# Performance work log

Measured on AMD Instinct MI355X. Metric: run time of the kernel, lower is better.

Reference implementation:

```python
import jax, jax.numpy as jnp
import numpy as np

B, T, D, Q = 32, 2048, 512, 512


def setup_inputs() -> dict:
    key = jax.random.key(0)
    k0, k1, k2, k3, k4, k5 = jax.random.split(key, 6)
    output_data = jax.random.normal(k0, (B, T, D), dtype=jnp.float32)
    query = jax.random.normal(k1, (B, Q), dtype=jnp.float32)
    # valid lengths in [1, T] so no row is fully masked
    lengths = jax.random.randint(k2, (B,), 1, T + 1).astype(jnp.int32)
    w = jax.random.normal(k3, (D, D), dtype=jnp.float32) * (1.0 / np.sqrt(D))
    u = jax.random.normal(k4, (D, Q), dtype=jnp.float32) * (1.0 / np.sqrt(Q))
    v = jax.random.normal(k5, (D, 1), dtype=jnp.float32)
    return {"output_data": output_data, "query": query, "lengths": lengths,
            "w": w, "u": u, "v": v}


def reference(output_data, query, lengths, w, u, v):
    # raw_score = W @ output + U @ query (broadcast over seq)   [B, T, D]
    raw = jnp.einsum('btd,ed->bte', output_data, w) \
        + jnp.einsum('bq,eq->be', query, u)[:, None, :]
    # score = tanh(raw) @ v                                     [B, T, 1]
    score = jnp.tanh(raw) @ v
    # additive mask: 0 on valid positions, -inf on padding
    valid = jnp.arange(T)[None, :] < lengths[:, None]           # [B, T]
    score = score + jnp.where(valid, 0.0, -jnp.inf)[:, :, None]
    weights = jax.nn.softmax(score, axis=1)                     # [B, T, 1]
    expectation = jnp.sum(weights * output_data, axis=1)        # [B, D]
    # dropout_rate=0.0 -> dropout is identity
    return score, weights, expectation
```

## Files before the change

kernel.cpp:

```cpp
#include <hip/hip_runtime.h>
#include <math.h>


#define TPB 256
constexpr int B = 32, T = 2048, D = 512, Qd = 512;
constexpr int NROW = B * T;
#define NEG_SENTINEL (-1e30f)

typedef __attribute__((ext_vector_type(8))) short bf16x8;
typedef __attribute__((ext_vector_type(4))) float f32x4;

__device__ __forceinline__ void lds_barrier() {
    asm volatile("s_waitcnt lgkmcnt(0)" ::: "memory");
    __builtin_amdgcn_s_barrier();
}

__device__ __forceinline__ unsigned cvtpk(float a, float b) {
    unsigned r;
    asm("v_cvt_pk_bf16_f32 %0, %1, %2" : "=v"(r) : "v"(a), "v"(b));
    return r;
}
__device__ __forceinline__ unsigned packsplit(float f0, float f1, unsigned& lopack) {
    unsigned hp = cvtpk(f0, f1);
    float h0 = __builtin_bit_cast(float, hp << 16);
    float h1 = __builtin_bit_cast(float, hp & 0xFFFF0000u);
    lopack = cvtpk(f0 - h0, f1 - h1);
    return hp;
}
__device__ __forceinline__ void cvt8(const float4 a, const float4 b, uint4& hi, uint4& lo) {
    hi.x = packsplit(a.x, a.y, lo.x);
    hi.y = packsplit(a.z, a.w, lo.y);
    hi.z = packsplit(b.x, b.y, lo.z);
    hi.w = packsplit(b.z, b.w, lo.w);
}
__device__ __forceinline__ float fast_tanh(float x) {
    float a = fabsf(x);
    float e = __expf(-2.f * a);
    float t = (1.f - e) / (1.f + e);
    return copysignf(t, x);
}

__global__ void k_uq(const float* __restrict__ query, const float* __restrict__ u,
                     float* __restrict__ uq) {
    int b = blockIdx.x;
    __shared__ float q_s[Qd];
    for (int i = threadIdx.x; i < Qd; i += TPB) q_s[i] = query[b * Qd + i];
    __syncthreads();
    for (int e = threadIdx.x; e < D; e += TPB) {
        const float4* urow = (const float4*)(u + (size_t)e * Qd);
        float acc = 0.f;
        for (int q4 = 0; q4 < Qd / 4; ++q4) {
            float4 uu = urow[q4];
            float4 qq = *(const float4*)(q_s + q4 * 4);
            acc += uu.x * qq.x + uu.y * qq.y + uu.z * qq.z + uu.w * qq.w;
        }
        uq[b * D + e] = acc;
    }
}

__global__ void k_convW(const float* __restrict__ W,
                        uint4* __restrict__ WhF, uint4* __restrict__ WlF) {
    const int g = blockIdx.x * 256 + threadIdx.x;
    const int e = g >> 6, s = g & 63;
    const float4* src = (const float4*)(W + (size_t)e * D + s * 8);
    float4 a = src[0], bq = src[1];
    uint4 hi, lo;
    cvt8(a, bq, hi, lo);
    const int nt = e >> 7, cb = (e >> 4) & 7, lo16 = e & 15;
    const int kc = s >> 2, hi4 = s & 3;
    const size_t idx = ((size_t)(nt * 16 + kc) * 8 + cb) * 64 + hi4 * 16 + lo16;
    WhF[idx] = hi;
    WlF[idx] = lo;
}

__global__ __launch_bounds__(256, 4) void k_gemm(
    const float* __restrict__ X,
    const uint4* __restrict__ WhF,
    const uint4* __restrict__ WlF,
    const float* __restrict__ v,
    const float* __restrict__ uqg,
    float* __restrict__ partialS)
{
    __shared__ uint4 Ah[2][4 * 128], Al[2][4 * 128];
    __shared__ float scr[2][128];

    const int gidx = blockIdx.x;
    const int logical = (gidx & 7) * 256 + (gidx >> 3);
    const int mt = logical >> 2, nt = logical & 3;
    const int row0 = mt * 128, e0 = nt * 128;
    const int b = row0 >> 11;

    const int tid = threadIdx.x, lane = tid & 63, wid = tid >> 6;
    const int wm = wid >> 1, wn = wid & 1;
    const int lo16 = lane & 15, hi4 = lane >> 4;
    const int arow = tid & 127, akh = tid >> 7;

    const float4* Xg = (const float4*)(X + (size_t)(row0 + arow) * D + akh * 16);
    const uint4* WhB = WhF + ((size_t)nt * 16) * 8 * 64 + (wn * 4) * 64 + lane;
    const uint4* WlB = WlF + ((size_t)nt * 16) * 8 * 64 + (wn * 4) * 64 + lane;

    f32x4 acc[4][4];
#pragma unroll
    for (int i = 0; i < 4; ++i)
#pragma unroll
        for (int j = 0; j < 4; ++j) acc[i][j] = (f32x4){0.f, 0.f, 0.f, 0.f};

    float4 xr[2][4];
#pragma unroll
    for (int i = 0; i < 4; ++i) xr[0][i] = Xg[i];
#pragma unroll
    for (int i = 0; i < 4; ++i) xr[1][i] = Xg[8 + i];
    {
        uint4 hp, lp;
        cvt8(xr[0][0], xr[0][1], hp, lp);
        Ah[0][(akh * 2 + 0) * 128 + arow] = hp;
        Al[0][(akh * 2 + 0) * 128 + arow] = lp;
        cvt8(xr[0][2], xr[0][3], hp, lp);
        Ah[0][(akh * 2 + 1) * 128 + arow] = hp;
        Al[0][(akh * 2 + 1) * 128 + arow] = lp;
    }

#pragma unroll
    for (int kc = 0; kc < 16; ++kc) {
        const int cur = kc & 1, nxt = cur ^ 1;
        lds_barrier();

        uint4 bhr[4], blr[4];
        {
            const uint4* wh = WhB + (size_t)kc * 8 * 64;
            const uint4* wl = WlB + (size_t)kc * 8 * 64;
#pragma unroll
            for (int fc = 0; fc < 4; ++fc) {
                bhr[fc] = wh[fc * 64];
                blr[fc] = wl[fc * 64];
            }
        }

        if (kc + 1 < 16) {
            uint4 hp, lp;
            cvt8(xr[nxt][0], xr[nxt][1], hp, lp);
            Ah[nxt][(akh * 2 + 0) * 128 + arow] = hp;
            Al[nxt][(akh * 2 + 0) * 128 + arow] = lp;
            cvt8(xr[nxt][2], xr[nxt][3], hp, lp);
            Ah[nxt][(akh * 2 + 1) * 128 + arow] = hp;
            Al[nxt][(akh * 2 + 1) * 128 + arow] = lp;
        }

        bf16x8 aH[4], aL[4];
#pragma unroll
        for (int fr = 0; fr < 4; ++fr) {
            const int idx = hi4 * 128 + wm * 64 + fr * 16 + lo16;
            aH[fr] = __builtin_bit_cast(bf16x8, Ah[cur][idx]);
            aL[fr] = __builtin_bit_cast(bf16x8, Al[cur][idx]);
        }

#pragma unroll
        for (int fc = 0; fc < 4; ++fc) {
            const bf16x8 bH = __builtin_bit_cast(bf16x8, bhr[fc]);
            const bf16x8 bL = __builtin_bit_cast(bf16x8, blr[fc]);
#pragma unroll
            for (int fr = 0; fr < 4; ++fr) {
                acc[fr][fc] = __builtin_amdgcn_mfma_f32_16x16x32_bf16(aH[fr], bH, acc[fr][fc], 0, 0, 0);
                acc[fr][fc] = __builtin_amdgcn_mfma_f32_16x16x32_bf16(aH[fr], bL, acc[fr][fc], 0, 0, 0);
                acc[fr][fc] = __builtin_amdgcn_mfma_f32_16x16x32_bf16(aL[fr], bH, acc[fr][fc], 0, 0, 0);
            }
        }

        if (kc + 2 < 16) {
#pragma unroll
            for (int i = 0; i < 4; ++i) xr[cur][i] = Xg[(kc + 2) * 8 + i];
        }
    }

    const int colbase = e0 + wn * 64;
#pragma unroll
    for (int fr = 0; fr < 4; ++fr) {
        float ps[4] = {0.f, 0.f, 0.f, 0.f};
#pragma unroll
        for (int fc = 0; fc < 4; ++fc) {
            const int col = colbase + fc * 16 + lo16;
            const float uqc = uqg[b * D + col];
            const float vc  = v[col];
#pragma unroll
            for (int i = 0; i < 4; ++i)
                ps[i] += fast_tanh(acc[fr][fc][i] + uqc) * vc;
        }
#pragma unroll
        for (int i = 0; i < 4; ++i) {
            float p = ps[i];
#pragma unroll
            for (int off = 8; off >= 1; off >>= 1) p += __shfl_xor(p, off, 16);
            if (lo16 == 0) scr[wn][wm * 64 + fr * 16 + hi4 * 4 + i] = p;
        }
    }
    __syncthreads();
    if (tid < 128)
        partialS[(size_t)nt * NROW + row0 + tid] = scr[0][tid] + scr[1][tid];
}

__global__ void k_combine(const float* __restrict__ partialS,
                          const int* __restrict__ lengths,
                          float* __restrict__ score) {
    const int i = blockIdx.x * TPB + threadIdx.x;
    const int b = i >> 11, t = i & (T - 1);
    float s = partialS[i] + partialS[NROW + i] + partialS[2 * NROW + i] + partialS[3 * NROW + i];
    score[i] = (t < lengths[b]) ? s : NEG_SENTINEL;
}

__global__ void k_softmax(const float* __restrict__ score, float* __restrict__ weights) {
    const int b = blockIdx.x;
    const float* s = score + (size_t)b * T;
    float m = -INFINITY;
    for (int t = threadIdx.x; t < T; t += TPB) m = fmaxf(m, s[t]);
#pragma unroll
    for (int off = 32; off >= 1; off >>= 1) m = fmaxf(m, __shfl_xor(m, off, 64));
    __shared__ float redm[4];
    if ((threadIdx.x & 63) == 0) redm[threadIdx.x >> 6] = m;
    __syncthreads();
    m = fmaxf(fmaxf(redm[0], redm[1]), fmaxf(redm[2], redm[3]));

    float sum = 0.f;
    for (int t = threadIdx.x; t < T; t += TPB) sum += __expf(s[t] - m);
#pragma unroll
    for (int off = 32; off >= 1; off >>= 1) sum += __shfl_xor(sum, off, 64);
    __shared__ float reds[4];
    if ((threadIdx.x & 63) == 0) reds[threadIdx.x >> 6] = sum;
    __syncthreads();
    const float inv = 1.f / (reds[0] + reds[1] + reds[2] + reds[3]);

    for (int t = threadIdx.x; t < T; t += TPB)
        weights[(size_t)b * T + t] = __expf(s[t] - m) * inv;
}

__global__ void k_exp_partial(const float* __restrict__ X, const float* __restrict__ wts,
                              float* __restrict__ part) {
    const int b = blockIdx.x >> 4;
    const int c = blockIdx.x & 15;
    const int t0 = c * 128;
    const int d0 = threadIdx.x * 4;
    const float* Xb = X + ((size_t)b * T + t0) * D + d0;
    const float* wb = wts + (size_t)b * T + t0;
    float4 a = {0.f, 0.f, 0.f, 0.f};
    for (int t = 0; t < 128; ++t) {
        const float wgt = wb[t];
        const float4 x = *(const float4*)(Xb + (size_t)t * D);
        a.x += wgt * x.x; a.y += wgt * x.y; a.z += wgt * x.z; a.w += wgt * x.w;
    }
    *(float4*)(part + ((size_t)(b * 16 + c)) * D + d0) = a;
}

__global__ void k_exp_reduce(const float* __restrict__ part, float* __restrict__ out) {
    const int i = blockIdx.x * TPB + threadIdx.x;
    const int b = i >> 9, d = i & 511;
    float a = 0.f;
#pragma unroll
    for (int c = 0; c < 16; ++c) a += part[((size_t)(b * 16 + c)) * D + d];
    out[i] = a;
}

extern "C" void kernel_launch(void* const* d_in, const int* in_sizes, int n_in,
                              void* d_out, int out_size, void* d_ws, size_t ws_size,
                              hipStream_t stream) {
    const float* X      = (const float*)d_in[0];
    const float* query  = (const float*)d_in[1];
    const int*   len    = (const int*)  d_in[2];
    const float* w      = (const float*)d_in[3];
    const float* u      = (const float*)d_in[4];
    const float* v      = (const float*)d_in[5];

    float* out     = (float*)d_out;
    float* score   = out;
    float* weights = out + (size_t)B * T;
    float* expec   = out + (size_t)2 * B * T;

    float* uq       = (float*)d_ws;
    float* partialS = uq + (size_t)B * D;
    uint4* WhF      = (uint4*)(partialS + (size_t)4 * NROW);
    uint4* WlF      = WhF + 32768;
    float* part     = partialS;

    k_uq         <<<B,            TPB, 0, stream>>>(query, u, uq);
    k_convW      <<<128,          TPB, 0, stream>>>(w, WhF, WlF);
    k_gemm       <<<2048,         TPB, 0, stream>>>(X, WhF, WlF, v, uq, partialS);
    k_combine    <<<NROW / TPB,   TPB, 0, stream>>>(partialS, len, score);
    k_softmax    <<<B,            TPB, 0, stream>>>(score, weights);
    k_exp_partial<<<B * 16,       128, 0, stream>>>(X, weights, part);
    k_exp_reduce <<<B * D / TPB,  TPB, 0, stream>>>(part, expec);
}
```

Baseline: 185.7 us.

## Stage W fragments through LDS with register prefetch and reorder MFMA pipeline

Each block now loads its W hi/lo tile for the next k-chunk cooperatively into registers, then writes it to shared memory after compute. Previously each wave read its own W fragments straight from global memory. A second barrier separates fragment reads from compute, the MFMAs are regrouped by product term, and s_setprio raises wave priority around the MFMA block. Launch bounds drop to 3 blocks per SM to make room for the extra registers and LDS, which costs occupancy and adds a barrier per iteration.

Result: slower. 326.8 us (+76.0%).

```diff
diff --git a/kernel.cpp b/kernel.cpp
--- a/kernel.cpp
+++ b/kernel.cpp
@@ -73,7 +73,7 @@
     WlF[idx] = lo;
 }
 
-__global__ __launch_bounds__(256, 4) void k_gemm(
+__global__ __launch_bounds__(256, 3) void k_gemm(
     const float* __restrict__ X,
     const uint4* __restrict__ WhF,
     const uint4* __restrict__ WlF,
@@ -82,6 +82,7 @@
     float* __restrict__ partialS)
 {
     __shared__ uint4 Ah[2][4 * 128], Al[2][4 * 128];
+    __shared__ uint4 Bh[8 * 64], Bl[8 * 64];
     __shared__ float scr[2][128];
 
     const int gidx = blockIdx.x;
@@ -96,8 +97,8 @@
     const int arow = tid & 127, akh = tid >> 7;
 
     const float4* Xg = (const float4*)(X + (size_t)(row0 + arow) * D + akh * 16);
-    const uint4* WhB = WhF + ((size_t)nt * 16) * 8 * 64 + (wn * 4) * 64 + lane;
-    const uint4* WlB = WlF + ((size_t)nt * 16) * 8 * 64 + (wn * 4) * 64 + lane;
+    const uint4* WhS = WhF + ((size_t)nt * 16) * 8 * 64 + tid;
+    const uint4* WlS = WlF + ((size_t)nt * 16) * 8 * 64 + tid;
 
     f32x4 acc[4][4];
 #pragma unroll
@@ -110,6 +111,9 @@
     for (int i = 0; i < 4; ++i) xr[0][i] = Xg[i];
 #pragma unroll
     for (int i = 0; i < 4; ++i) xr[1][i] = Xg[8 + i];
+    uint4 bs0, bs1, bs2, bs3;
+    bs0 = WhS[0];  bs1 = WhS[256];
+    bs2 = WlS[0];  bs3 = WlS[256];
     {
         uint4 hp, lp;
         cvt8(xr[0][0], xr[0][1], hp, lp);
@@ -119,21 +123,37 @@
         Ah[0][(akh * 2 + 1) * 128 + arow] = hp;
         Al[0][(akh * 2 + 1) * 128 + arow] = lp;
     }
+    Bh[tid] = bs0;  Bh[tid + 256] = bs1;
+    Bl[tid] = bs2;  Bl[tid + 256] = bs3;
 
 #pragma unroll
     for (int kc = 0; kc < 16; ++kc) {
         const int cur = kc & 1, nxt = cur ^ 1;
         lds_barrier();
 
-        uint4 bhr[4], blr[4];
-        {
-            const uint4* wh = WhB + (size_t)kc * 8 * 64;
-            const uint4* wl = WlB + (size_t)kc * 8 * 64;
-#pragma unroll
-            for (int fc = 0; fc < 4; ++fc) {
-                bhr[fc] = wh[fc * 64];
-                blr[fc] = wl[fc * 64];
-            }
+        bf16x8 aH[4], aL[4], bH[4], bL[4];
+#pragma unroll
+        for (int fr = 0; fr < 4; ++fr) {
+            const int idx = hi4 * 128 + wm * 64 + fr * 16 + lo16;
+            aH[fr] = __builtin_bit_cast(bf16x8, Ah[cur][idx]);
+            aL[fr] = __builtin_bit_cast(bf16x8, Al[cur][idx]);
+        }
+#pragma unroll
+        for (int fc = 0; fc < 4; ++fc) {
+            const int idx = (wn * 4 + fc) * 64 + lane;
+            bH[fc] = __builtin_bit_cast(bf16x8, Bh[idx]);
+            bL[fc] = __builtin_bit_cast(bf16x8, Bl[idx]);
+        }
+
+        if (kc + 1 < 16) {
+            const uint4* wh = WhS + (size_t)(kc + 1) * 512;
+            const uint4* wl = WlS + (size_t)(kc + 1) * 512;
+            bs0 = wh[0];  bs1 = wh[256];
+            bs2 = wl[0];  bs3 = wl[256];
+        }
+        if (kc + 2 < 16) {
+#pragma unroll
+            for (int i = 0; i < 4; ++i) xr[cur][i] = Xg[(kc + 2) * 8 + i];
         }
 
         if (kc + 1 < 16) {
@@ -146,29 +166,29 @@
             Al[nxt][(akh * 2 + 1) * 128 + arow] = lp;
         }
 
-        bf16x8 aH[4], aL[4];
-#pragma unroll
-        for (int fr = 0; fr < 4; ++fr) {
-            const int idx = hi4 * 128 + wm * 64 + fr * 16 + lo16;
-            aH[fr] = __builtin_bit_cast(bf16x8, Ah[cur][idx]);
-            aL[fr] = __builtin_bit_cast(bf16x8, Al[cur][idx]);
-        }
-
-#pragma unroll
-        for (int fc = 0; fc < 4; ++fc) {
-            const bf16x8 bH = __builtin_bit_cast(bf16x8, bhr[fc]);
-            const bf16x8 bL = __builtin_bit_cast(bf16x8, blr[fc]);
-#pragma unroll
-            for (int fr = 0; fr < 4; ++fr) {
-                acc[fr][fc] = __builtin_amdgcn_mfma_f32_16x16x32_bf16(aH[fr], bH, acc[fr][fc], 0, 0, 0);
-                acc[fr][fc] = __builtin_amdgcn_mfma_f32_16x16x32_bf16(aH[fr], bL, acc[fr][fc], 0, 0, 0);
-                acc[fr][fc] = __builtin_amdgcn_mfma_f32_16x16x32_bf16(aL[fr], bH, acc[fr][fc], 0, 0, 0);
-            }
-        }
-
-        if (kc + 2 < 16) {
-#pragma unroll
-            for (int i = 0; i < 4; ++i) xr[cur][i] = Xg[(kc + 2) * 8 + i];
+        lds_barrier();
+
+        __builtin_amdgcn_s_setprio(1);
+#pragma unroll
+        for (int fc = 0; fc < 4; ++fc)
+#pragma unroll
+            for (int fr = 0; fr < 4; ++fr)
+                acc[fr][fc] = __builtin_amdgcn_mfma_f32_16x16x32_bf16(aH[fr], bH[fc], acc[fr][fc], 0, 0, 0);
+#pragma unroll
+        for (int fc = 0; fc < 4; ++fc)
+#pragma unroll
+            for (int fr = 0; fr < 4; ++fr)
+                acc[fr][fc] = __builtin_amdgcn_mfma_f32_16x16x32_bf16(aH[fr], bL[fc], acc[fr][fc], 0, 0, 0);
+#pragma unroll
+        for (int fc = 0; fc < 4; ++fc)
+#pragma unroll
+            for (int fr = 0; fr < 4; ++fr)
+                acc[fr][fc] = __builtin_amdgcn_mfma_f32_16x16x32_bf16(aL[fr], bH[fc], acc[fr][fc], 0, 0, 0);
+        __builtin_amdgcn_s_setprio(0);
+
+        if (kc + 1 < 16) {
+            Bh[tid] = bs0;  Bh[tid + 256] = bs1;
+            Bl[tid] = bs2;  Bl[tid + 256] = bs3;
         }
     }
 
```

## Pre-split X into bf16 hi/lo fragment layout and stream GEMM from registers

Applied to the files above, without the earlier changes.

Adds a conversion kernel that splits X into bf16 hi/lo parts and stores them in MFMA fragment order in workspace. A new GEMM kernel then loads A and B fragments straight from global memory into double-buffered registers, with no LDS staging. The aim is to remove the in-GEMM conversion and the LDS traffic and barriers. In exchange it writes and rereads a 128 MB intermediate for X, and occupancy drops to 2 blocks per CU. The new path runs only if the workspace is large enough, otherwise the old kernel is used.

Result: slower. 205.9 us (+10.9%).

```diff
diff --git a/kernel.cpp b/kernel.cpp
--- a/kernel.cpp
+++ b/kernel.cpp
@@ -73,6 +73,114 @@
     WlF[idx] = lo;
 }
 
+__global__ void k_convX(const float* __restrict__ X,
+                        uint4* __restrict__ XhF, uint4* __restrict__ XlF) {
+    const int g = blockIdx.x * 256 + threadIdx.x;
+    const int lo16 = g & 15, hi4 = (g >> 4) & 3, rb = (g >> 6) & 7;
+    const int kc = (g >> 9) & 15, mt = g >> 13;
+    const int row = mt * 128 + rb * 16 + lo16;
+    const int d0 = kc * 32 + hi4 * 8;
+    const float4* src = (const float4*)(X + (size_t)row * D + d0);
+    float4 a = src[0], bq = src[1];
+    uint4 hi, lo;
+    cvt8(a, bq, hi, lo);
+    XhF[g] = hi;
+    XlF[g] = lo;
+}
+
+__global__ __launch_bounds__(256, 2) void k_gemm_stream(
+    const uint4* __restrict__ XhF, const uint4* __restrict__ XlF,
+    const uint4* __restrict__ WhF, const uint4* __restrict__ WlF,
+    const float* __restrict__ v,
+    const float* __restrict__ uqg,
+    float* __restrict__ partialS)
+{
+    __shared__ float scr[2][128];
+
+    const int gidx = blockIdx.x;
+    const int logical = (gidx & 7) * 256 + (gidx >> 3);
+    const int mt = logical >> 2, nt = logical & 3;
+    const int row0 = mt * 128, e0 = nt * 128;
+    const int b = row0 >> 11;
+
+    const int tid = threadIdx.x, lane = tid & 63, wid = tid >> 6;
+    const int wm = wid >> 1, wn = wid & 1;
+    const int lo16 = lane & 15, hi4 = lane >> 4;
+
+    const uint4* XhB = XhF + ((size_t)mt * 16) * 8 * 64 + (wm * 4) * 64 + lane;
+    const uint4* XlB = XlF + ((size_t)mt * 16) * 8 * 64 + (wm * 4) * 64 + lane;
+    const uint4* WhB = WhF + ((size_t)nt * 16) * 8 * 64 + (wn * 4) * 64 + lane;
+    const uint4* WlB = WlF + ((size_t)nt * 16) * 8 * 64 + (wn * 4) * 64 + lane;
+
+    f32x4 acc[4][4];
+#pragma unroll
+    for (int i = 0; i < 4; ++i)
+#pragma unroll
+        for (int j = 0; j < 4; ++j) acc[i][j] = (f32x4){0.f, 0.f, 0.f, 0.f};
+
+    uint4 ah[2][4], al[2][4], bh[2][4], bl[2][4];
+#pragma unroll
+    for (int f = 0; f < 4; ++f) {
+        ah[0][f] = XhB[f * 64];
+        al[0][f] = XlB[f * 64];
+        bh[0][f] = WhB[f * 64];
+        bl[0][f] = WlB[f * 64];
+    }
+
+#pragma unroll
+    for (int kc = 0; kc < 16; ++kc) {
+        const int cur = kc & 1, nxt = cur ^ 1;
+        if (kc + 1 < 16) {
+            const size_t off = (size_t)(kc + 1) * 512;
+#pragma unroll
+            for (int f = 0; f < 4; ++f) {
+                ah[nxt][f] = XhB[off + f * 64];
+                al[nxt][f] = XlB[off + f * 64];
+                bh[nxt][f] = WhB[off + f * 64];
+                bl[nxt][f] = WlB[off + f * 64];
+            }
+        }
+#pragma unroll
+        for (int fc = 0; fc < 4; ++fc) {
+            const bf16x8 bH = __builtin_bit_cast(bf16x8, bh[cur][fc]);
+            const bf16x8 bL = __builtin_bit_cast(bf16x8, bl[cur][fc]);
+#pragma unroll
+            for (int fr = 0; fr < 4; ++fr) {
+                const bf16x8 aH = __builtin_bit_cast(bf16x8, ah[cur][fr]);
+                const bf16x8 aL = __builtin_bit_cast(bf16x8, al[cur][fr]);
+                acc[fr][fc] = __builtin_amdgcn_mfma_f32_16x16x32_bf16(aH, bH, acc[fr][fc], 0, 0, 0);
+                acc[fr][fc] = __builtin_amdgcn_mfma_f32_16x16x32_bf16(aH, bL, acc[fr][fc], 0, 0, 0);
+                acc[fr][fc] = __builtin_amdgcn_mfma_f32_16x16x32_bf16(aL, bH, acc[fr][fc], 0, 0, 0);
+            }
+        }
+    }
+
+    const int colbase = e0 + wn * 64;
+#pragma unroll
+    for (int fr = 0; fr < 4; ++fr) {
+        float ps[4] = {0.f, 0.f, 0.f, 0.f};
+#pragma unroll
+        for (int fc = 0; fc < 4; ++fc) {
+            const int col = colbase + fc * 16 + lo16;
+            const float uqc = uqg[b * D + col];
+            const float vc  = v[col];
+#pragma unroll
+            for (int i = 0; i < 4; ++i)
+                ps[i] += fast_tanh(acc[fr][fc][i] + uqc) * vc;
+        }
+#pragma unroll
+        for (int i = 0; i < 4; ++i) {
+            float p = ps[i];
+#pragma unroll
+            for (int off = 8; off >= 1; off >>= 1) p += __shfl_xor(p, off, 16);
+            if (lo16 == 0) scr[wn][wm * 64 + fr * 16 + hi4 * 4 + i] = p;
+        }
+    }
+    __syncthreads();
+    if (tid < 128)
+        partialS[(size_t)nt * NROW + row0 + tid] = scr[0][tid] + scr[1][tid];
+}
+
 __global__ __launch_bounds__(256, 4) void k_gemm(
     const float* __restrict__ X,
     const uint4* __restrict__ WhF,
@@ -277,11 +385,21 @@
     float* partialS = uq + (size_t)B * D;
     uint4* WhF      = (uint4*)(partialS + (size_t)4 * NROW);
     uint4* WlF      = WhF + 32768;
+    uint4* XhF      = WlF + 32768;
+    uint4* XlF      = XhF + (size_t)NROW * 64;
     float* part     = partialS;
+
+    const size_t WS_FAST = (size_t)65536 + 1048576 + 2 * 524288 + 2 * 67108864;
+    const bool fast = ws_size >= WS_FAST;
 
     k_uq         <<<B,            TPB, 0, stream>>>(query, u, uq);
     k_convW      <<<128,          TPB, 0, stream>>>(w, WhF, WlF);
-    k_gemm       <<<2048,         TPB, 0, stream>>>(X, WhF, WlF, v, uq, partialS);
+    if (fast) {
+        k_convX      <<<NROW * 64 / TPB, TPB, 0, stream>>>(X, XhF, XlF);
+        k_gemm_stream<<<2048,            TPB, 0, stream>>>(XhF, XlF, WhF, WlF, v, uq, partialS);
+    } else {
+        k_gemm       <<<2048,            TPB, 0, stream>>>(X, WhF, WlF, v, uq, partialS);
+    }
     k_combine    <<<NROW / TPB,   TPB, 0, stream>>>(partialS, len, score);
     k_softmax    <<<B,            TPB, 0, stream>>>(score, weights);
     k_exp_partial<<<B * 16,       128, 0, stream>>>(X, weights, part);
```
